# Kernel tuning notes

Measured on AMD Instinct MI355X. Metric: run time of the kernel, lower is better.

## Reference

```python
import jax, jax.numpy as jnp
import numpy as np

TWO_PI = 2.0 * np.pi
LN_EPS = 1e-5


def _periods(out_dim, nb):
    # periods[i,j,g] = i*(out_dim*nb) + j*nb + g + 2
    return jnp.arange(out_dim * out_dim * nb, dtype=jnp.float32).reshape(out_dim, out_dim, nb) + 2.0


def _layer(x, M, gamma, beta, P, residual):
    # x: (B,S,in), M: (out,in), P: (out,out,nb)
    out_dim, _, nb = P.shape
    S = x.shape[1]
    xt = jnp.matmul(x, M.T)  # (B,S,out)
    mu = jnp.mean(xt, axis=-1, keepdims=True)
    var = jnp.mean((xt - mu) ** 2, axis=-1, keepdims=True)
    xn = (xt - mu) / jnp.sqrt(var + LN_EPS) * gamma + beta
    pos = jnp.arange(S, dtype=jnp.float32)[:, None, None, None]  # (S,1,1,1)
    phi = jnp.cos(TWO_PI * pos / _periods(out_dim, nb)[None])  # (S,out,out,nb)
    W = jnp.einsum('ijg,sijg->sij', P, phi)  # (S,out,out) contract basis first
    Nk = jnp.einsum('bsj,sij->bsi', xn, W)  # (B,S,out)
    return Nk + residual


def setup_inputs() -> dict:
    key = jax.random.key(0)
    ks = jax.random.split(key, 8)
    B, S, D_in, D, NB = 8, 1024, 64, 96, 8
    u = lambda k, shape, a: jax.random.uniform(k, shape, jnp.float32, -a, a)
    return {
        'seq': jax.random.normal(ks[0], (B, S, D_in), jnp.float32),
        'M1': u(ks[1], (D, D_in), 0.5),
        'P1': u(ks[2], (D, D, NB), 0.1),
        'Wres1': u(ks[3], (D, D_in), 0.1),
        'g1': jnp.ones((D,), jnp.float32),
        'b1': jnp.zeros((D,), jnp.float32),
        'M2': u(ks[4], (D, D), 0.5),
        'P2': u(ks[5], (D, D, NB), 0.1),
        'g2': jnp.ones((D,), jnp.float32),
        'b2': jnp.zeros((D,), jnp.float32),
    }


def reference(seq, M1, P1, Wres1, g1, b1, M2, P2, g2, b2):
    # Layer 1: 64 -> 96, 'separate' residual uses a Linear projection
    x1 = _layer(seq, M1, g1, b1, P1, jnp.matmul(seq, Wres1.T))
    # Layer 2: 96 -> 96, 'separate' residual with in_dim==out_dim is Identity
    x2 = _layer(x1, M2, g2, b2, P2, x1)
    return x2
```

## Files before the change

kernel.cpp:

```cpp
#include <hip/hip_runtime.h>
#include <hip/hip_fp16.h>

#define S_LEN    1024
#define B_SZ     8
#define D_IN     64
#define D_OUT    96
#define NB       8
#define NE       (D_OUT * D_OUT)
#define CHUNK    32
#define NCHUNK   (S_LEN / CHUNK)
#define NT_W     256
#define NWBLK    (NCHUNK * (NE / NT_W))
#define NT_C     512
#define HPAD     104
#define SPAD     100
#define XPAD     68

__device__ __forceinline__ float cos_rev(float v) {
    v -= floorf(v);
    return __builtin_amdgcn_cosf(v);
}

__global__ void __launch_bounds__(NT_W)
w_kernel(const float* __restrict__ P1, const float* __restrict__ P2,
         __half* __restrict__ W1, __half* __restrict__ W2) {
    const int c  = blockIdx.x / (NE / NT_W);
    const int eb = blockIdx.x % (NE / NT_W);
    const int e  = eb * NT_W + threadIdx.x;
    const int s0 = c * CHUNK;
    const float s0f = (float)s0;

    float p1l[NB], p2l[NB];
    *(float4*)&p1l[0] = *(const float4*)(P1 + e * NB);
    *(float4*)&p1l[4] = *(const float4*)(P1 + e * NB + 4);
    *(float4*)&p2l[0] = *(const float4*)(P2 + e * NB);
    *(float4*)&p2l[4] = *(const float4*)(P2 + e * NB + 4);

    float cc[NB], cp[NB], kk[NB];
    #pragma unroll
    for (int g = 0; g < NB; ++g) {
        const float inv = __builtin_amdgcn_rcpf((float)(e * NB + 2 + g));
        cc[g] = cos_rev(s0f * inv);
        cp[g] = cos_rev((s0f - 1.0f) * inv);
        kk[g] = 2.0f * __builtin_amdgcn_cosf(inv);
    }

    #pragma unroll 4
    for (int s = s0; s < s0 + CHUNK; ++s) {
        float a1 = 0.0f, a2 = 0.0f;
        #pragma unroll
        for (int g = 0; g < NB; ++g) {
            a1 = fmaf(p1l[g], cc[g], a1);
            a2 = fmaf(p2l[g], cc[g], a2);
        }
        W1[s * NE + e] = __float2half(a1);
        W2[s * NE + e] = __float2half(a2);
        #pragma unroll
        for (int g = 0; g < NB; ++g) {
            float cn = fmaf(kk[g], cc[g], -cp[g]);
            cp[g] = cc[g];
            cc[g] = cn;
        }
    }
}

__device__ __forceinline__ void nkdot2(const __half* __restrict__ w0,
                                       const __half* __restrict__ w1,
                                       const float* __restrict__ xr,
                                       float& a0, float& a1) {
    #pragma unroll
    for (int h = 0; h < 2; ++h) {
        #pragma unroll
        for (int j = h * 6; j < h * 6 + 6; ++j) {
            float4 xa = *(const float4*)(xr + 8 * j);
            float4 xb = *(const float4*)(xr + 8 * j + 4);
            float4 r0 = *(const float4*)(w0 + 8 * j);
            float4 r1 = *(const float4*)(w1 + 8 * j);
            const __half2* h0 = (const __half2*)&r0;
            const __half2* h1 = (const __half2*)&r1;
            float2 c;
            c = __half22float2(h0[0]); a0 = fmaf(c.x, xa.x, a0); a0 = fmaf(c.y, xa.y, a0);
            c = __half22float2(h0[1]); a0 = fmaf(c.x, xa.z, a0); a0 = fmaf(c.y, xa.w, a0);
            c = __half22float2(h0[2]); a0 = fmaf(c.x, xb.x, a0); a0 = fmaf(c.y, xb.y, a0);
            c = __half22float2(h0[3]); a0 = fmaf(c.x, xb.z, a0); a0 = fmaf(c.y, xb.w, a0);
            c = __half22float2(h1[0]); a1 = fmaf(c.x, xa.x, a1); a1 = fmaf(c.y, xa.y, a1);
            c = __half22float2(h1[1]); a1 = fmaf(c.x, xa.z, a1); a1 = fmaf(c.y, xa.w, a1);
            c = __half22float2(h1[2]); a1 = fmaf(c.x, xb.x, a1); a1 = fmaf(c.y, xb.y, a1);
            c = __half22float2(h1[3]); a1 = fmaf(c.x, xb.z, a1); a1 = fmaf(c.y, xb.w, a1);
        }
    }
}

__device__ __forceinline__ void stage_W(__half* __restrict__ wh,
                                        const __half* __restrict__ Wg,
                                        int tid) {
    for (int cidx = tid; cidx < NE / 8; cidx += NT_C) {
        const int i = cidx / 12;
        const int j = (cidx % 12) * 8;
        *(float4*)(wh + i * HPAD + j) = *(const float4*)(Wg + cidx * 8);
    }
}

__global__ void __launch_bounds__(NT_C)
consumer(const float* __restrict__ seq,
         const float* __restrict__ M1, const float* __restrict__ Wres1,
         const float* __restrict__ M2,
         const float* __restrict__ g1, const float* __restrict__ b1,
         const float* __restrict__ g2, const float* __restrict__ b2,
         const __half* __restrict__ W1g, const __half* __restrict__ W2g,
         float* __restrict__ out) {
    __shared__ __align__(16) __half wh [D_OUT * HPAD];
    __shared__ __align__(16) float  xn [B_SZ * SPAD];
    __shared__ __align__(16) float  x1b[B_SZ * SPAD];
    __shared__ __align__(16) float  rsb[B_SZ * SPAD];

    const int s   = blockIdx.x;
    const int tid = threadIdx.x;

    {
        int b = tid >> 6, k = tid & 63;
        x1b[b * SPAD + k] = seq[((size_t)b * S_LEN + s) * D_IN + k];
    }
    __syncthreads();

    stage_W(wh, W1g + (size_t)s * NE, tid);

    for (int pass = 0; pass < 2; ++pass) {
        int idx = tid + pass * NT_C;
        if (idx >= B_SZ * D_OUT) break;
        int i = idx >> 3, b = idx & 7;
        const float4* m  = (const float4*)(M1 + i * D_IN);
        const float4* wr = (const float4*)(Wres1 + i * D_IN);
        const float*  xr = x1b + b * SPAD;
        float at = 0.0f, ar = 0.0f;
        #pragma unroll
        for (int k = 0; k < D_IN / 4; ++k) {
            float4 mv = m[k], rv = wr[k];
            float x0 = xr[4*k], x1 = xr[4*k+1], x2 = xr[4*k+2], x3 = xr[4*k+3];
            at = fmaf(mv.x, x0, fmaf(mv.y, x1, fmaf(mv.z, x2, fmaf(mv.w, x3, at))));
            ar = fmaf(rv.x, x0, fmaf(rv.y, x1, fmaf(rv.z, x2, fmaf(rv.w, x3, ar))));
        }
        xn [b * SPAD + i] = at;
        rsb[b * SPAD + i] = ar;
    }
    __syncthreads();

    {
        const int b = tid >> 6, lane = tid & 63;
        const bool lo = (lane < 32);
        float* row = xn + b * SPAD;
        float v0 = row[lane];
        float v1 = lo ? row[64 + lane] : 0.0f;
        float sum = v0 + v1, sq = fmaf(v0, v0, v1 * v1);
        #pragma unroll
        for (int off = 32; off > 0; off >>= 1) {
            sum += __shfl_down(sum, off, 64);
            sq  += __shfl_down(sq,  off, 64);
        }
        sum = __shfl(sum, 0, 64);
        sq  = __shfl(sq,  0, 64);
        const float mu  = sum * (1.0f / 96.0f);
        const float var = fmaf(sq, 1.0f / 96.0f, -(mu * mu));
        const float rs  = rsqrtf(var + 1e-5f);
        row[lane] = fmaf((v0 - mu) * rs, g1[lane], b1[lane]);
        if (lo) row[64 + lane] = fmaf((v1 - mu) * rs, g1[64 + lane], b1[64 + lane]);
    }
    __syncthreads();

    if (tid < 8 * 48) {
        const int b  = tid & 7;
        const int ip = tid >> 3;
        float a0 = 0.0f, a1 = 0.0f;
        nkdot2(wh + ip * HPAD, wh + (ip + 48) * HPAD, xn + b * SPAD, a0, a1);
        x1b[b * SPAD + ip]      = rsb[b * SPAD + ip]      + a0;
        x1b[b * SPAD + ip + 48] = rsb[b * SPAD + ip + 48] + a1;
    }
    __syncthreads();

    stage_W(wh, W2g + (size_t)s * NE, tid);

    for (int pass = 0; pass < 2; ++pass) {
        int idx = tid + pass * NT_C;
        if (idx >= B_SZ * D_OUT) break;
        int i = idx >> 3, b = idx & 7;
        const float4* m  = (const float4*)(M2 + i * D_OUT);
        const float*  xr = x1b + b * SPAD;
        float at = 0.0f;
        #pragma unroll
        for (int k = 0; k < D_OUT / 4; ++k) {
            float4 mv = m[k];
            at = fmaf(mv.x, xr[4*k], fmaf(mv.y, xr[4*k+1],
                 fmaf(mv.z, xr[4*k+2], fmaf(mv.w, xr[4*k+3], at))));
        }
        xn[b * SPAD + i] = at;
    }
    __syncthreads();

    {
        const int b = tid >> 6, lane = tid & 63;
        const bool lo = (lane < 32);
        float* row = xn + b * SPAD;
        float v0 = row[lane];
        float v1 = lo ? row[64 + lane] : 0.0f;
        float sum = v0 + v1, sq = fmaf(v0, v0, v1 * v1);
        #pragma unroll
        for (int off = 32; off > 0; off >>= 1) {
            sum += __shfl_down(sum, off, 64);
            sq  += __shfl_down(sq,  off, 64);
        }
        sum = __shfl(sum, 0, 64);
        sq  = __shfl(sq,  0, 64);
        const float mu  = sum * (1.0f / 96.0f);
        const float var = fmaf(sq, 1.0f / 96.0f, -(mu * mu));
        const float rs  = rsqrtf(var + 1e-5f);
        row[lane] = fmaf((v0 - mu) * rs, g2[lane], b2[lane]);
        if (lo) row[64 + lane] = fmaf((v1 - mu) * rs, g2[64 + lane], b2[64 + lane]);
    }
    __syncthreads();

    if (tid < 8 * 48) {
        const int b  = tid & 7;
        const int ip = tid >> 3;
        float a0 = 0.0f, a1 = 0.0f;
        nkdot2(wh + ip * HPAD, wh + (ip + 48) * HPAD, xn + b * SPAD, a0, a1);
        const size_t base = ((size_t)b * S_LEN + s) * D_OUT;
        out[base + ip]      = a0 + x1b[b * SPAD + ip];
        out[base + ip + 48] = a1 + x1b[b * SPAD + ip + 48];
    }
}

__global__ void __launch_bounds__(NT_W)
hier_fallback(const float* __restrict__ seq,  const float* __restrict__ M1,
              const float* __restrict__ P1,   const float* __restrict__ Wres1,
              const float* __restrict__ g1,   const float* __restrict__ b1,
              const float* __restrict__ M2,   const float* __restrict__ P2,
              const float* __restrict__ g2,   const float* __restrict__ b2,
              float* __restrict__ out) {
    __shared__ __align__(16) float w[D_OUT * SPAD];
    __shared__ __align__(16) float xin[B_SZ * XPAD];
    __shared__ __align__(16) float xn [B_SZ * SPAD];
    __shared__ __align__(16) float x1b[B_SZ * SPAD];
    const int s = blockIdx.x, tid = threadIdx.x;
    const float sf = (float)s;

    for (int idx = tid; idx < B_SZ * D_IN; idx += NT_W) {
        int b = idx >> 6, k = idx & (D_IN - 1);
        xin[b * XPAD + k] = seq[(b * S_LEN + s) * D_IN + k];
    }
    for (int e = tid; e < NE; e += NT_W) {
        float pl[8];
        *(float4*)&pl[0] = *(const float4*)(P1 + e * NB);
        *(float4*)&pl[4] = *(const float4*)(P1 + e * NB + 4);
        float acc = 0.0f;
        #pragma unroll
        for (int g = 0; g < NB; ++g) {
            float v = sf * __builtin_amdgcn_rcpf((float)(e * NB + 2 + g));
            acc = fmaf(pl[g], cos_rev(v), acc);
        }
        int i = e / D_OUT;
        w[e + (SPAD - D_OUT) * i] = acc;
    }
    __syncthreads();
    for (int idx = tid; idx < B_SZ * D_OUT; idx += NT_W) {
        int i = idx >> 3, b = idx & 7;
        const float4* m  = (const float4*)(M1 + i * D_IN);
        const float4* wr = (const float4*)(Wres1 + i * D_IN);
        const float*  xr = xin + b * XPAD;
        float at = 0.0f, ar = 0.0f;
        #pragma unroll
        for (int k = 0; k < D_IN / 4; ++k) {
            float4 mv = m[k], rv = wr[k];
            float x0 = xr[4*k], x1 = xr[4*k+1], x2 = xr[4*k+2], x3 = xr[4*k+3];
            at = fmaf(mv.x, x0, fmaf(mv.y, x1, fmaf(mv.z, x2, fmaf(mv.w, x3, at))));
            ar = fmaf(rv.x, x0, fmaf(rv.y, x1, fmaf(rv.z, x2, fmaf(rv.w, x3, ar))));
        }
        xn [b * SPAD + i] = at;
        x1b[b * SPAD + i] = ar;
    }
    __syncthreads();
    {
        const int b = tid >> 5, rr = tid & 31;
        float* row = xn + b * SPAD;
        float v0 = row[rr], v1 = row[rr + 32], v2 = row[rr + 64];
        float sum = v0 + v1 + v2, sq = fmaf(v0, v0, fmaf(v1, v1, v2 * v2));
        #pragma unroll
        for (int off = 16; off > 0; off >>= 1) {
            sum += __shfl_down(sum, off, 32);
            sq  += __shfl_down(sq,  off, 32);
        }
        sum = __shfl(sum, 0, 32); sq = __shfl(sq, 0, 32);
        float mu = sum * (1.0f/96.0f), var = fmaf(sq, 1.0f/96.0f, -(mu*mu));
        float rs = rsqrtf(var + 1e-5f);
        row[rr]      = fmaf((v0 - mu) * rs, g1[rr],      b1[rr]);
        row[rr + 32] = fmaf((v1 - mu) * rs, g1[rr + 32], b1[rr + 32]);
        row[rr + 64] = fmaf((v2 - mu) * rs, g1[rr + 64], b1[rr + 64]);
    }
    __syncthreads();
    for (int idx = tid; idx < B_SZ * D_OUT; idx += NT_W) {
        int i = idx >> 3, b = idx & 7;
        const float* wrow = w + i * SPAD;
        const float* xr   = xn + b * SPAD;
        float acc = 0.0f;
        #pragma unroll
        for (int j = 0; j < D_OUT / 4; ++j) {
            float4 wv = *(const float4*)(wrow + 4 * j);
            float4 xv = *(const float4*)(xr + 4 * j);
            acc = fmaf(wv.x, xv.x, fmaf(wv.y, xv.y, fmaf(wv.z, xv.z, fmaf(wv.w, xv.w, acc))));
        }
        x1b[b * SPAD + i] += acc;
    }
    __syncthreads();
    for (int e = tid; e < NE; e += NT_W) {
        float pl[8];
        *(float4*)&pl[0] = *(const float4*)(P2 + e * NB);
        *(float4*)&pl[4] = *(const float4*)(P2 + e * NB + 4);
        float acc = 0.0f;
        #pragma unroll
        for (int g = 0; g < NB; ++g) {
            float v = sf * __builtin_amdgcn_rcpf((float)(e * NB + 2 + g));
            acc = fmaf(pl[g], cos_rev(v), acc);
        }
        int i = e / D_OUT;
        w[e + (SPAD - D_OUT) * i] = acc;
    }
    for (int idx = tid; idx < B_SZ * D_OUT; idx += NT_W) {
        int i = idx >> 3, b = idx & 7;
        const float4* m  = (const float4*)(M2 + i * D_OUT);
        const float*  xr = x1b + b * SPAD;
        float at = 0.0f;
        #pragma unroll
        for (int k = 0; k < D_OUT / 4; ++k) {
            float4 mv = m[k];
            at = fmaf(mv.x, xr[4*k], fmaf(mv.y, xr[4*k+1],
                 fmaf(mv.z, xr[4*k+2], fmaf(mv.w, xr[4*k+3], at))));
        }
        xn[b * SPAD + i] = at;
    }
    __syncthreads();
    {
        const int b = tid >> 5, rr = tid & 31;
        float* row = xn + b * SPAD;
        float v0 = row[rr], v1 = row[rr + 32], v2 = row[rr + 64];
        float sum = v0 + v1 + v2, sq = fmaf(v0, v0, fmaf(v1, v1, v2 * v2));
        #pragma unroll
        for (int off = 16; off > 0; off >>= 1) {
            sum += __shfl_down(sum, off, 32);
            sq  += __shfl_down(sq,  off, 32);
        }
        sum = __shfl(sum, 0, 32); sq = __shfl(sq, 0, 32);
        float mu = sum * (1.0f/96.0f), var = fmaf(sq, 1.0f/96.0f, -(mu*mu));
        float rs = rsqrtf(var + 1e-5f);
        row[rr]      = fmaf((v0 - mu) * rs, g2[rr],      b2[rr]);
        row[rr + 32] = fmaf((v1 - mu) * rs, g2[rr + 32], b2[rr + 32]);
        row[rr + 64] = fmaf((v2 - mu) * rs, g2[rr + 64], b2[rr + 64]);
    }
    __syncthreads();
    for (int idx = tid; idx < B_SZ * D_OUT; idx += NT_W) {
        int i = idx >> 3, b = idx & 7;
        const float* wrow = w + i * SPAD;
        const float* xr   = xn + b * SPAD;
        float acc = 0.0f;
        #pragma unroll
        for (int j = 0; j < D_OUT / 4; ++j) {
            float4 wv = *(const float4*)(wrow + 4 * j);
            float4 xv = *(const float4*)(xr + 4 * j);
            acc = fmaf(wv.x, xv.x, fmaf(wv.y, xv.y, fmaf(wv.z, xv.z, fmaf(wv.w, xv.w, acc))));
        }
        out[(b * S_LEN + s) * D_OUT + i] = acc + x1b[b * SPAD + i];
    }
}

extern "C" void kernel_launch(void* const* d_in, const int* in_sizes, int n_in,
                              void* d_out, int out_size, void* d_ws, size_t ws_size,
                              hipStream_t stream) {
    const float* seq   = (const float*)d_in[0];
    const float* M1    = (const float*)d_in[1];
    const float* P1    = (const float*)d_in[2];
    const float* Wres1 = (const float*)d_in[3];
    const float* g1    = (const float*)d_in[4];
    const float* b1    = (const float*)d_in[5];
    const float* M2    = (const float*)d_in[6];
    const float* P2    = (const float*)d_in[7];
    const float* g2    = (const float*)d_in[8];
    const float* b2    = (const float*)d_in[9];
    float* out = (float*)d_out;

    const size_t need = (size_t)2 * S_LEN * NE * sizeof(__half);
    if (ws_size >= need) {
        __half* W1 = (__half*)d_ws;
        __half* W2 = W1 + (size_t)S_LEN * NE;
        w_kernel<<<dim3(NWBLK), dim3(NT_W), 0, stream>>>(P1, P2, W1, W2);
        consumer<<<dim3(S_LEN), dim3(NT_C), 0, stream>>>(
            seq, M1, Wres1, M2, g1, b1, g2, b2, W1, W2, out);
    } else {
        hier_fallback<<<dim3(S_LEN), dim3(NT_W), 0, stream>>>(
            seq, M1, P1, Wres1, g1, b1, M2, P2, g2, b2, out);
    }
}
```

Measured before the change: 118.4 us.

## Generate per-position W in shared memory inside consumer, drop precompute kernel

Removes the separate kernel that precomputed fp16 W1/W2 for every position into workspace, along with the fallback kernel. Each consumer block now computes its own W rows directly into shared memory from P using cosine evaluations. This avoids writing and re-reading about 38 MB of workspace and one kernel launch. In exchange it gives up the Chebyshev recurrence, so every element costs 8 cos and 8 rcp calls inside the consumer.

```diff
diff --git a/kernel.cpp b/kernel.cpp
--- a/kernel.cpp
+++ b/kernel.cpp
@@ -7,60 +7,33 @@
 #define D_OUT    96
 #define NB       8
 #define NE       (D_OUT * D_OUT)
-#define CHUNK    32
-#define NCHUNK   (S_LEN / CHUNK)
-#define NT_W     256
-#define NWBLK    (NCHUNK * (NE / NT_W))
 #define NT_C     512
 #define HPAD     104
 #define SPAD     100
-#define XPAD     68
 
 __device__ __forceinline__ float cos_rev(float v) {
     v -= floorf(v);
     return __builtin_amdgcn_cosf(v);
 }
 
-__global__ void __launch_bounds__(NT_W)
-w_kernel(const float* __restrict__ P1, const float* __restrict__ P2,
-         __half* __restrict__ W1, __half* __restrict__ W2) {
-    const int c  = blockIdx.x / (NE / NT_W);
-    const int eb = blockIdx.x % (NE / NT_W);
-    const int e  = eb * NT_W + threadIdx.x;
-    const int s0 = c * CHUNK;
-    const float s0f = (float)s0;
-
-    float p1l[NB], p2l[NB];
-    *(float4*)&p1l[0] = *(const float4*)(P1 + e * NB);
-    *(float4*)&p1l[4] = *(const float4*)(P1 + e * NB + 4);
-    *(float4*)&p2l[0] = *(const float4*)(P2 + e * NB);
-    *(float4*)&p2l[4] = *(const float4*)(P2 + e * NB + 4);
-
-    float cc[NB], cp[NB], kk[NB];
-    #pragma unroll
-    for (int g = 0; g < NB; ++g) {
-        const float inv = __builtin_amdgcn_rcpf((float)(e * NB + 2 + g));
-        cc[g] = cos_rev(s0f * inv);
-        cp[g] = cos_rev((s0f - 1.0f) * inv);
-        kk[g] = 2.0f * __builtin_amdgcn_cosf(inv);
-    }
-
-    #pragma unroll 4
-    for (int s = s0; s < s0 + CHUNK; ++s) {
-        float a1 = 0.0f, a2 = 0.0f;
+__device__ __forceinline__ void gen_W(__half* __restrict__ wh,
+                                      const float* __restrict__ P,
+                                      float sf, int tid) {
+    #pragma unroll 3
+    for (int k = 0; k < NE / NT_C; ++k) {
+        const int e = tid + k * NT_C;
+        float pl[NB];
+        *(float4*)&pl[0] = *(const float4*)(P + e * NB);
+        *(float4*)&pl[4] = *(const float4*)(P + e * NB + 4);
+        float acc = 0.0f;
         #pragma unroll
         for (int g = 0; g < NB; ++g) {
-            a1 = fmaf(p1l[g], cc[g], a1);
-            a2 = fmaf(p2l[g], cc[g], a2);
-        }
-        W1[s * NE + e] = __float2half(a1);
-        W2[s * NE + e] = __float2half(a2);
-        #pragma unroll
-        for (int g = 0; g < NB; ++g) {
-            float cn = fmaf(kk[g], cc[g], -cp[g]);
-            cp[g] = cc[g];
-            cc[g] = cn;
-        }
+            const float inv = __builtin_amdgcn_rcpf((float)(e * NB + 2 + g));
+            acc = fmaf(pl[g], cos_rev(sf * inv), acc);
+        }
+        const int i = (unsigned)e / D_OUT;
+        const int j = (unsigned)e % D_OUT;
+        wh[i * HPAD + j] = __float2half(acc);
     }
 }
 
@@ -91,24 +64,14 @@
     }
 }
 
-__device__ __forceinline__ void stage_W(__half* __restrict__ wh,
-                                        const __half* __restrict__ Wg,
-                                        int tid) {
-    for (int cidx = tid; cidx < NE / 8; cidx += NT_C) {
-        const int i = cidx / 12;
-        const int j = (cidx % 12) * 8;
-        *(float4*)(wh + i * HPAD + j) = *(const float4*)(Wg + cidx * 8);
-    }
-}
-
 __global__ void __launch_bounds__(NT_C)
-consumer(const float* __restrict__ seq,
-         const float* __restrict__ M1, const float* __restrict__ Wres1,
-         const float* __restrict__ M2,
-         const float* __restrict__ g1, const float* __restrict__ b1,
-         const float* __restrict__ g2, const float* __restrict__ b2,
-         const __half* __restrict__ W1g, const __half* __restrict__ W2g,
-         float* __restrict__ out) {
+consumer_direct(const float* __restrict__ seq,
+                const float* __restrict__ M1, const float* __restrict__ Wres1,
+                const float* __restrict__ M2,
+                const float* __restrict__ g1, const float* __restrict__ b1,
+                const float* __restrict__ g2, const float* __restrict__ b2,
+                const float* __restrict__ P1, const float* __restrict__ P2,
+                float* __restrict__ out) {
     __shared__ __align__(16) __half wh [D_OUT * HPAD];
     __shared__ __align__(16) float  xn [B_SZ * SPAD];
     __shared__ __align__(16) float  x1b[B_SZ * SPAD];
@@ -116,14 +79,14 @@
 
     const int s   = blockIdx.x;
     const int tid = threadIdx.x;
+    const float sf = (float)s;
 
     {
         int b = tid >> 6, k = tid & 63;
         x1b[b * SPAD + k] = seq[((size_t)b * S_LEN + s) * D_IN + k];
     }
-    __syncthreads();
-
-    stage_W(wh, W1g + (size_t)s * NE, tid);
+    gen_W(wh, P1, sf, tid);
+    __syncthreads();
 
     for (int pass = 0; pass < 2; ++pass) {
         int idx = tid + pass * NT_C;
@@ -177,7 +140,7 @@
     }
     __syncthreads();
 
-    stage_W(wh, W2g + (size_t)s * NE, tid);
+    gen_W(wh, P2, sf, tid);
 
     for (int pass = 0; pass < 2; ++pass) {
         int idx = tid + pass * NT_C;
@@ -226,147 +189,6 @@
         const size_t base = ((size_t)b * S_LEN + s) * D_OUT;
         out[base + ip]      = a0 + x1b[b * SPAD + ip];
         out[base + ip + 48] = a1 + x1b[b * SPAD + ip + 48];
-    }
-}
-
-__global__ void __launch_bounds__(NT_W)
-hier_fallback(const float* __restrict__ seq,  const float* __restrict__ M1,
-              const float* __restrict__ P1,   const float* __restrict__ Wres1,
-              const float* __restrict__ g1,   const float* __restrict__ b1,
-              const float* __restrict__ M2,   const float* __restrict__ P2,
-              const float* __restrict__ g2,   const float* __restrict__ b2,
-              float* __restrict__ out) {
-    __shared__ __align__(16) float w[D_OUT * SPAD];
-    __shared__ __align__(16) float xin[B_SZ * XPAD];
-    __shared__ __align__(16) float xn [B_SZ * SPAD];
-    __shared__ __align__(16) float x1b[B_SZ * SPAD];
-    const int s = blockIdx.x, tid = threadIdx.x;
-    const float sf = (float)s;
-
-    for (int idx = tid; idx < B_SZ * D_IN; idx += NT_W) {
-        int b = idx >> 6, k = idx & (D_IN - 1);
-        xin[b * XPAD + k] = seq[(b * S_LEN + s) * D_IN + k];
-    }
-    for (int e = tid; e < NE; e += NT_W) {
-        float pl[8];
-        *(float4*)&pl[0] = *(const float4*)(P1 + e * NB);
-        *(float4*)&pl[4] = *(const float4*)(P1 + e * NB + 4);
-        float acc = 0.0f;
-        #pragma unroll
-        for (int g = 0; g < NB; ++g) {
-            float v = sf * __builtin_amdgcn_rcpf((float)(e * NB + 2 + g));
-            acc = fmaf(pl[g], cos_rev(v), acc);
-        }
-        int i = e / D_OUT;
-        w[e + (SPAD - D_OUT) * i] = acc;
-    }
-    __syncthreads();
-    for (int idx = tid; idx < B_SZ * D_OUT; idx += NT_W) {
-        int i = idx >> 3, b = idx & 7;
-        const float4* m  = (const float4*)(M1 + i * D_IN);
-        const float4* wr = (const float4*)(Wres1 + i * D_IN);
-        const float*  xr = xin + b * XPAD;
-        float at = 0.0f, ar = 0.0f;
-        #pragma unroll
-        for (int k = 0; k < D_IN / 4; ++k) {
-            float4 mv = m[k], rv = wr[k];
-            float x0 = xr[4*k], x1 = xr[4*k+1], x2 = xr[4*k+2], x3 = xr[4*k+3];
-            at = fmaf(mv.x, x0, fmaf(mv.y, x1, fmaf(mv.z, x2, fmaf(mv.w, x3, at))));
-            ar = fmaf(rv.x, x0, fmaf(rv.y, x1, fmaf(rv.z, x2, fmaf(rv.w, x3, ar))));
-        }
-        xn [b * SPAD + i] = at;
-        x1b[b * SPAD + i] = ar;
-    }
-    __syncthreads();
-    {
-        const int b = tid >> 5, rr = tid & 31;
-        float* row = xn + b * SPAD;
-        float v0 = row[rr], v1 = row[rr + 32], v2 = row[rr + 64];
-        float sum = v0 + v1 + v2, sq = fmaf(v0, v0, fmaf(v1, v1, v2 * v2));
-        #pragma unroll
-        for (int off = 16; off > 0; off >>= 1) {
-            sum += __shfl_down(sum, off, 32);
-            sq  += __shfl_down(sq,  off, 32);
-        }
-        sum = __shfl(sum, 0, 32); sq = __shfl(sq, 0, 32);
-        float mu = sum * (1.0f/96.0f), var = fmaf(sq, 1.0f/96.0f, -(mu*mu));
-        float rs = rsqrtf(var + 1e-5f);
-        row[rr]      = fmaf((v0 - mu) * rs, g1[rr],      b1[rr]);
-        row[rr + 32] = fmaf((v1 - mu) * rs, g1[rr + 32], b1[rr + 32]);
-        row[rr + 64] = fmaf((v2 - mu) * rs, g1[rr + 64], b1[rr + 64]);
-    }
-    __syncthreads();
-    for (int idx = tid; idx < B_SZ * D_OUT; idx += NT_W) {
-        int i = idx >> 3, b = idx & 7;
-        const float* wrow = w + i * SPAD;
-        const float* xr   = xn + b * SPAD;
-        float acc = 0.0f;
-        #pragma unroll
-        for (int j = 0; j < D_OUT / 4; ++j) {
-            float4 wv = *(const float4*)(wrow + 4 * j);
-            float4 xv = *(const float4*)(xr + 4 * j);
-            acc = fmaf(wv.x, xv.x, fmaf(wv.y, xv.y, fmaf(wv.z, xv.z, fmaf(wv.w, xv.w, acc))));
-        }
-        x1b[b * SPAD + i] += acc;
-    }
-    __syncthreads();
-    for (int e = tid; e < NE; e += NT_W) {
-        float pl[8];
-        *(float4*)&pl[0] = *(const float4*)(P2 + e * NB);
-        *(float4*)&pl[4] = *(const float4*)(P2 + e * NB + 4);
-        float acc = 0.0f;
-        #pragma unroll
-        for (int g = 0; g < NB; ++g) {
-            float v = sf * __builtin_amdgcn_rcpf((float)(e * NB + 2 + g));
-            acc = fmaf(pl[g], cos_rev(v), acc);
-        }
-        int i = e / D_OUT;
-        w[e + (SPAD - D_OUT) * i] = acc;
-    }
-    for (int idx = tid; idx < B_SZ * D_OUT; idx += NT_W) {
-        int i = idx >> 3, b = idx & 7;
-        const float4* m  = (const float4*)(M2 + i * D_OUT);
-        const float*  xr = x1b + b * SPAD;
-        float at = 0.0f;
-        #pragma unroll
-        for (int k = 0; k < D_OUT / 4; ++k) {
-            float4 mv = m[k];
-            at = fmaf(mv.x, xr[4*k], fmaf(mv.y, xr[4*k+1],
-                 fmaf(mv.z, xr[4*k+2], fmaf(mv.w, xr[4*k+3], at))));
-        }
-        xn[b * SPAD + i] = at;
-    }
-    __syncthreads();
-    {
-        const int b = tid >> 5, rr = tid & 31;
-        float* row = xn + b * SPAD;
-        float v0 = row[rr], v1 = row[rr + 32], v2 = row[rr + 64];
-        float sum = v0 + v1 + v2, sq = fmaf(v0, v0, fmaf(v1, v1, v2 * v2));
-        #pragma unroll
-        for (int off = 16; off > 0; off >>= 1) {
-            sum += __shfl_down(sum, off, 32);
-            sq  += __shfl_down(sq,  off, 32);
-        }
-        sum = __shfl(sum, 0, 32); sq = __shfl(sq, 0, 32);
-        float mu = sum * (1.0f/96.0f), var = fmaf(sq, 1.0f/96.0f, -(mu*mu));
-        float rs = rsqrtf(var + 1e-5f);
-        row[rr]      = fmaf((v0 - mu) * rs, g2[rr],      b2[rr]);
-        row[rr + 32] = fmaf((v1 - mu) * rs, g2[rr + 32], b2[rr + 32]);
-        row[rr + 64] = fmaf((v2 - mu) * rs, g2[rr + 64], b2[rr + 64]);
-    }
-    __syncthreads();
-    for (int idx = tid; idx < B_SZ * D_OUT; idx += NT_W) {
-        int i = idx >> 3, b = idx & 7;
-        const float* wrow = w + i * SPAD;
-        const float* xr   = xn + b * SPAD;
-        float acc = 0.0f;
-        #pragma unroll
-        for (int j = 0; j < D_OUT / 4; ++j) {
-            float4 wv = *(const float4*)(wrow + 4 * j);
-            float4 xv = *(const float4*)(xr + 4 * j);
-            acc = fmaf(wv.x, xv.x, fmaf(wv.y, xv.y, fmaf(wv.z, xv.z, fmaf(wv.w, xv.w, acc))));
-        }
-        out[(b * S_LEN + s) * D_OUT + i] = acc + x1b[b * SPAD + i];
     }
 }
 
@@ -384,16 +206,8 @@
     const float* g2    = (const float*)d_in[8];
     const float* b2    = (const float*)d_in[9];
     float* out = (float*)d_out;
-
-    const size_t need = (size_t)2 * S_LEN * NE * sizeof(__half);
-    if (ws_size >= need) {
-        __half* W1 = (__half*)d_ws;
-        __half* W2 = W1 + (size_t)S_LEN * NE;
-        w_kernel<<<dim3(NWBLK), dim3(NT_W), 0, stream>>>(P1, P2, W1, W2);
-        consumer<<<dim3(S_LEN), dim3(NT_C), 0, stream>>>(
-            seq, M1, Wres1, M2, g1, b1, g2, b2, W1, W2, out);
-    } else {
-        hier_fallback<<<dim3(S_LEN), dim3(NT_W), 0, stream>>>(
-            seq, M1, P1, Wres1, g1, b1, M2, P2, g2, b2, out);
-    }
-}
+    (void)d_ws; (void)ws_size;
+
+    consumer_direct<<<dim3(S_LEN), dim3(NT_C), 0, stream>>>(
+        seq, M1, Wres1, M2, g1, b1, g2, b2, P1, P2, out);
+}
```

Result: slower. 134.6 us (+13.7%).

## Process two elements per thread in W kernel and remap blocks to XCDs

Applied to the files above, without the earlier changes.

The W-generation kernel now gives each thread two adjacent elements and writes packed half2 stores, halving the block count and widening stores. Both kernels remap blockIdx so that each chunk of consecutive sequence positions lands on one XCD (blockIdx & 7). The intent is for the W data written by a producer chunk to stay in the same XCD's L2 when the consumer reads it. This doubles register use per thread in the W kernel, which may lower occupancy.

```diff
diff --git a/kernel.cpp b/kernel.cpp
--- a/kernel.cpp
+++ b/kernel.cpp
@@ -10,7 +10,10 @@
 #define CHUNK    32
 #define NCHUNK   (S_LEN / CHUNK)
 #define NT_W     256
-#define NWBLK    (NCHUNK * (NE / NT_W))
+#define EPT      2
+#define ESPAN    (NT_W * EPT)
+#define NSLICE   (NE / ESPAN)
+#define NWBLK    (NCHUNK * NSLICE)
 #define NT_C     512
 #define HPAD     104
 #define SPAD     100
@@ -24,42 +27,52 @@
 __global__ void __launch_bounds__(NT_W)
 w_kernel(const float* __restrict__ P1, const float* __restrict__ P2,
          __half* __restrict__ W1, __half* __restrict__ W2) {
-    const int c  = blockIdx.x / (NE / NT_W);
-    const int eb = blockIdx.x % (NE / NT_W);
-    const int e  = eb * NT_W + threadIdx.x;
+    const int x  = blockIdx.x & 7;
+    const int q  = blockIdx.x >> 3;
+    const int c  = x + 8 * (q / NSLICE);
+    const int eb = q % NSLICE;
+    const int e0 = eb * ESPAN + EPT * threadIdx.x;
     const int s0 = c * CHUNK;
     const float s0f = (float)s0;
 
-    float p1l[NB], p2l[NB];
-    *(float4*)&p1l[0] = *(const float4*)(P1 + e * NB);
-    *(float4*)&p1l[4] = *(const float4*)(P1 + e * NB + 4);
-    *(float4*)&p2l[0] = *(const float4*)(P2 + e * NB);
-    *(float4*)&p2l[4] = *(const float4*)(P2 + e * NB + 4);
-
-    float cc[NB], cp[NB], kk[NB];
+    float p1l[EPT][NB], p2l[EPT][NB], cc[EPT][NB], cp[EPT][NB], kk[EPT][NB];
     #pragma unroll
-    for (int g = 0; g < NB; ++g) {
-        const float inv = __builtin_amdgcn_rcpf((float)(e * NB + 2 + g));
-        cc[g] = cos_rev(s0f * inv);
-        cp[g] = cos_rev((s0f - 1.0f) * inv);
-        kk[g] = 2.0f * __builtin_amdgcn_cosf(inv);
-    }
-
-    #pragma unroll 4
+    for (int ee = 0; ee < EPT; ++ee) {
+        *(float4*)&p1l[ee][0] = *(const float4*)(P1 + (e0 + ee) * NB);
+        *(float4*)&p1l[ee][4] = *(const float4*)(P1 + (e0 + ee) * NB + 4);
+        *(float4*)&p2l[ee][0] = *(const float4*)(P2 + (e0 + ee) * NB);
+        *(float4*)&p2l[ee][4] = *(const float4*)(P2 + (e0 + ee) * NB + 4);
+        #pragma unroll
+        for (int g = 0; g < NB; ++g) {
+            const float inv = __builtin_amdgcn_rcpf((float)((e0 + ee) * NB + 2 + g));
+            cc[ee][g] = cos_rev(s0f * inv);
+            cp[ee][g] = cos_rev((s0f - 1.0f) * inv);
+            kk[ee][g] = 2.0f * __builtin_amdgcn_cosf(inv);
+        }
+    }
+
+    #pragma unroll 2
     for (int s = s0; s < s0 + CHUNK; ++s) {
-        float a1 = 0.0f, a2 = 0.0f;
-        #pragma unroll
-        for (int g = 0; g < NB; ++g) {
-            a1 = fmaf(p1l[g], cc[g], a1);
-            a2 = fmaf(p2l[g], cc[g], a2);
-        }
-        W1[s * NE + e] = __float2half(a1);
-        W2[s * NE + e] = __float2half(a2);
-        #pragma unroll
-        for (int g = 0; g < NB; ++g) {
-            float cn = fmaf(kk[g], cc[g], -cp[g]);
-            cp[g] = cc[g];
-            cc[g] = cn;
+        float a1[EPT], a2[EPT];
+        #pragma unroll
+        for (int ee = 0; ee < EPT; ++ee) {
+            a1[ee] = 0.0f; a2[ee] = 0.0f;
+            #pragma unroll
+            for (int g = 0; g < NB; ++g) {
+                a1[ee] = fmaf(p1l[ee][g], cc[ee][g], a1[ee]);
+                a2[ee] = fmaf(p2l[ee][g], cc[ee][g], a2[ee]);
+            }
+        }
+        *(__half2*)(W1 + s * NE + e0) = __floats2half2_rn(a1[0], a1[1]);
+        *(__half2*)(W2 + s * NE + e0) = __floats2half2_rn(a2[0], a2[1]);
+        #pragma unroll
+        for (int ee = 0; ee < EPT; ++ee) {
+            #pragma unroll
+            for (int g = 0; g < NB; ++g) {
+                float cn = fmaf(kk[ee][g], cc[ee][g], -cp[ee][g]);
+                cp[ee][g] = cc[ee][g];
+                cc[ee][g] = cn;
+            }
         }
     }
 }
@@ -114,7 +127,9 @@
     __shared__ __align__(16) float  x1b[B_SZ * SPAD];
     __shared__ __align__(16) float  rsb[B_SZ * SPAD];
 
-    const int s   = blockIdx.x;
+    const int x = blockIdx.x & 7;
+    const int y = blockIdx.x >> 3;
+    const int s = ((x + 8 * (y >> 5)) << 5) + (y & 31);
     const int tid = threadIdx.x;
 
     {
```

After: 119.2 us. About the same (+0.7%).

## Fuse W generation and consumer into one persistent kernel with per-chunk flags

Applied to the files above, without the earlier changes.

Merges the separate W-producer kernel and the consumer kernel into one launch. Blocks take ordered tickets from an atomic counter: the first tickets generate W chunks and bump a per-chunk flag, and later tickets act as consumers that spin until their chunk's flag is complete. This lets consumer work overlap producer work and removes the kernel boundary, at the cost of a memset launch, atomic spin-waits, and producer blocks now using 512 threads instead of 256.

```diff
diff --git a/kernel.cpp b/kernel.cpp
--- a/kernel.cpp
+++ b/kernel.cpp
@@ -9,59 +9,18 @@
 #define NE       (D_OUT * D_OUT)
 #define CHUNK    32
 #define NCHUNK   (S_LEN / CHUNK)
+#define NT_C     512
+#define WPB      (NE / NT_C)
+#define NWBLK_F  (NCHUNK * WPB)
 #define NT_W     256
-#define NWBLK    (NCHUNK * (NE / NT_W))
-#define NT_C     512
 #define HPAD     104
 #define SPAD     100
 #define XPAD     68
+#define FLAG_STRIDE 16
 
 __device__ __forceinline__ float cos_rev(float v) {
     v -= floorf(v);
     return __builtin_amdgcn_cosf(v);
-}
-
-__global__ void __launch_bounds__(NT_W)
-w_kernel(const float* __restrict__ P1, const float* __restrict__ P2,
-         __half* __restrict__ W1, __half* __restrict__ W2) {
-    const int c  = blockIdx.x / (NE / NT_W);
-    const int eb = blockIdx.x % (NE / NT_W);
-    const int e  = eb * NT_W + threadIdx.x;
-    const int s0 = c * CHUNK;
-    const float s0f = (float)s0;
-
-    float p1l[NB], p2l[NB];
-    *(float4*)&p1l[0] = *(const float4*)(P1 + e * NB);
-    *(float4*)&p1l[4] = *(const float4*)(P1 + e * NB + 4);
-    *(float4*)&p2l[0] = *(const float4*)(P2 + e * NB);
-    *(float4*)&p2l[4] = *(const float4*)(P2 + e * NB + 4);
-
-    float cc[NB], cp[NB], kk[NB];
-    #pragma unroll
-    for (int g = 0; g < NB; ++g) {
-        const float inv = __builtin_amdgcn_rcpf((float)(e * NB + 2 + g));
-        cc[g] = cos_rev(s0f * inv);
-        cp[g] = cos_rev((s0f - 1.0f) * inv);
-        kk[g] = 2.0f * __builtin_amdgcn_cosf(inv);
-    }
-
-    #pragma unroll 4
-    for (int s = s0; s < s0 + CHUNK; ++s) {
-        float a1 = 0.0f, a2 = 0.0f;
-        #pragma unroll
-        for (int g = 0; g < NB; ++g) {
-            a1 = fmaf(p1l[g], cc[g], a1);
-            a2 = fmaf(p2l[g], cc[g], a2);
-        }
-        W1[s * NE + e] = __float2half(a1);
-        W2[s * NE + e] = __float2half(a2);
-        #pragma unroll
-        for (int g = 0; g < NB; ++g) {
-            float cn = fmaf(kk[g], cc[g], -cp[g]);
-            cp[g] = cc[g];
-            cc[g] = cn;
-        }
-    }
 }
 
 __device__ __forceinline__ void nkdot2(const __half* __restrict__ w0,
@@ -101,25 +60,83 @@
     }
 }
 
-__global__ void __launch_bounds__(NT_C)
-consumer(const float* __restrict__ seq,
-         const float* __restrict__ M1, const float* __restrict__ Wres1,
-         const float* __restrict__ M2,
-         const float* __restrict__ g1, const float* __restrict__ b1,
-         const float* __restrict__ g2, const float* __restrict__ b2,
-         const __half* __restrict__ W1g, const __half* __restrict__ W2g,
-         float* __restrict__ out) {
+__global__ void __launch_bounds__(NT_C, 1)
+fused(const float* __restrict__ seq,
+      const float* __restrict__ M1, const float* __restrict__ Wres1,
+      const float* __restrict__ M2,
+      const float* __restrict__ g1, const float* __restrict__ b1,
+      const float* __restrict__ g2, const float* __restrict__ b2,
+      const float* __restrict__ P1, const float* __restrict__ P2,
+      __half* __restrict__ W1g, __half* __restrict__ W2g,
+      int* __restrict__ flags,
+      float* __restrict__ out) {
     __shared__ __align__(16) __half wh [D_OUT * HPAD];
     __shared__ __align__(16) float  xn [B_SZ * SPAD];
     __shared__ __align__(16) float  x1b[B_SZ * SPAD];
     __shared__ __align__(16) float  rsb[B_SZ * SPAD];
-
-    const int s   = blockIdx.x;
+    __shared__ int s_ticket;
+
     const int tid = threadIdx.x;
+    if (tid == 0) s_ticket = atomicAdd(flags + 32 * FLAG_STRIDE, 1);
+    __syncthreads();
+    const int t = s_ticket;
+
+    if (t < NWBLK_F) {
+        const int c  = t / WPB;
+        const int eb = t % WPB;
+        const int e  = eb * NT_C + tid;
+        const int s0 = c * CHUNK;
+        const float s0f = (float)s0;
+
+        float p1l[NB], p2l[NB];
+        *(float4*)&p1l[0] = *(const float4*)(P1 + e * NB);
+        *(float4*)&p1l[4] = *(const float4*)(P1 + e * NB + 4);
+        *(float4*)&p2l[0] = *(const float4*)(P2 + e * NB);
+        *(float4*)&p2l[4] = *(const float4*)(P2 + e * NB + 4);
+
+        float cc[NB], cp[NB], kk[NB];
+        #pragma unroll
+        for (int g = 0; g < NB; ++g) {
+            const float inv = __builtin_amdgcn_rcpf((float)(e * NB + 2 + g));
+            cc[g] = cos_rev(s0f * inv);
+            cp[g] = cos_rev((s0f - 1.0f) * inv);
+            kk[g] = 2.0f * __builtin_amdgcn_cosf(inv);
+        }
+
+        #pragma unroll 4
+        for (int s = s0; s < s0 + CHUNK; ++s) {
+            float a1 = 0.0f, a2 = 0.0f;
+            #pragma unroll
+            for (int g = 0; g < NB; ++g) {
+                a1 = fmaf(p1l[g], cc[g], a1);
+                a2 = fmaf(p2l[g], cc[g], a2);
+            }
+            W1g[s * NE + e] = __float2half(a1);
+            W2g[s * NE + e] = __float2half(a2);
+            #pragma unroll
+            for (int g = 0; g < NB; ++g) {
+                float cn = fmaf(kk[g], cc[g], -cp[g]);
+                cp[g] = cc[g];
+                cc[g] = cn;
+            }
+        }
+        __threadfence();
+        __syncthreads();
+        if (tid == 0) atomicAdd(flags + c * FLAG_STRIDE, 1);
+        return;
+    }
+
+    const int s = t - NWBLK_F;
+    const int c = s >> 5;
 
     {
         int b = tid >> 6, k = tid & 63;
         x1b[b * SPAD + k] = seq[((size_t)b * S_LEN + s) * D_IN + k];
+    }
+    if (tid == 0) {
+        while (atomicAdd(flags + c * FLAG_STRIDE, 0) < WPB)
+            __builtin_amdgcn_s_sleep(16);
+        __threadfence();
     }
     __syncthreads();
 
@@ -385,13 +402,15 @@
     const float* b2    = (const float*)d_in[9];
     float* out = (float*)d_out;
 
-    const size_t need = (size_t)2 * S_LEN * NE * sizeof(__half);
-    if (ws_size >= need) {
-        __half* W1 = (__half*)d_ws;
-        __half* W2 = W1 + (size_t)S_LEN * NE;
-        w_kernel<<<dim3(NWBLK), dim3(NT_W), 0, stream>>>(P1, P2, W1, W2);
-        consumer<<<dim3(S_LEN), dim3(NT_C), 0, stream>>>(
-            seq, M1, Wres1, M2, g1, b1, g2, b2, W1, W2, out);
+    const size_t wbytes = (size_t)2 * S_LEN * NE * sizeof(__half);
+    const size_t flagsz = (size_t)(33 * FLAG_STRIDE) * sizeof(int);
+    if (ws_size >= wbytes + 4096) {
+        __half* W1   = (__half*)d_ws;
+        __half* W2   = W1 + (size_t)S_LEN * NE;
+        int*   flags = (int*)((char*)d_ws + wbytes);
+        hipMemsetAsync(flags, 0, flagsz, stream);
+        fused<<<dim3(NWBLK_F + S_LEN), dim3(NT_C), 0, stream>>>(
+            seq, M1, Wres1, M2, g1, b1, g2, b2, P1, P2, W1, W2, flags, out);
     } else {
         hier_fallback<<<dim3(S_LEN), dim3(NT_W), 0, stream>>>(
             seq, M1, P1, Wres1, g1, b1, M2, P2, g2, b2, out);
```

New measurement: 304.1 us. 2.57x slower.
